# Performance work log

Measured on AMD Instinct MI355X. Metric: run time of the kernel, lower is better.

## Reference

```python
import jax, jax.numpy as jnp
import numpy as np

E = 192; Q = 48; H = 3; HD = Q // H  # per-branch embed 48, 3 heads of 16
CONV_CH = 4; K = 15; PAD = K // 2


def layer_norm(x, g, b, eps=1e-6):
    m = jnp.mean(x, axis=-1, keepdims=True)
    v = jnp.mean((x - m) ** 2, axis=-1, keepdims=True)
    return (x - m) * jax.lax.rsqrt(v + eps) * g + b


def mha(x, w_in, b_in, w_o, b_o):
    # x: [B,S,48]; torch nn.MultiheadAttention math (dropout=eval/identity)
    B, S, _ = x.shape
    qkv = x @ w_in.T + b_in                      # [B,S,144]
    q, k, v = jnp.split(qkv, 3, axis=-1)
    q = q.reshape(B, S, H, HD)
    k = k.reshape(B, S, H, HD)
    v = v.reshape(B, S, H, HD)
    scores = jnp.einsum('bqhd,bkhd->bhqk', q, k) / jnp.sqrt(jnp.float32(HD))
    attn = jax.nn.softmax(scores, axis=-1)
    out = jnp.einsum('bhqk,bkhd->bqhd', attn, v).reshape(B, S, Q)
    return out @ w_o.T + b_o


def light_conv(x96, conv_w):
    # x96: [B,S,96] -> view(-1, 4, 96), depthwise conv1d (k=15, pad=7), view back
    B, S, W = x96.shape
    r = x96.reshape(-1, CONV_CH, W)              # [B*S/... wait: B*S*96/(4*96)=B*S/4? No: reshape(-1,4,96) => [B*S, ...]
    y = jax.lax.conv_general_dilated(
        r, conv_w, window_strides=(1,), padding=[(PAD, PAD)],
        dimension_numbers=('NCH', 'OIH', 'NCH'), feature_group_count=CONV_CH)
    return y.reshape(B, S, W)


def setup_inputs() -> dict:
    key = jax.random.key(0)
    ks = jax.random.split(key, 16)
    sc = 0.05
    d = {
        'x': jax.random.normal(ks[0], (128, 512, E), dtype=jnp.float32),
        'ln1_g': jnp.ones((E,), jnp.float32), 'ln1_b': jnp.zeros((E,), jnp.float32),
        'acc_wqkv': jax.random.normal(ks[1], (3 * Q, Q), jnp.float32) * sc,
        'acc_bqkv': jnp.zeros((3 * Q,), jnp.float32),
        'acc_wo': jax.random.normal(ks[2], (Q, Q), jnp.float32) * sc,
        'acc_bo': jnp.zeros((Q,), jnp.float32),
        'gyro_wqkv': jax.random.normal(ks[3], (3 * Q, Q), jnp.float32) * sc,
        'gyro_bqkv': jnp.zeros((3 * Q,), jnp.float32),
        'gyro_wo': jax.random.normal(ks[4], (Q, Q), jnp.float32) * sc,
        'gyro_bo': jnp.zeros((Q,), jnp.float32),
        'conv_w': jax.random.normal(ks[5], (CONV_CH, 1, K), jnp.float32) * sc,
        'ln2_g': jnp.ones((E,), jnp.float32), 'ln2_b': jnp.zeros((E,), jnp.float32),
        'w1': jax.random.normal(ks[6], (2 * E, E), jnp.float32) * sc,
        'b1': jnp.zeros((2 * E,), jnp.float32),
        'w2': jax.random.normal(ks[7], (E, 2 * E), jnp.float32) * sc,
        'b2': jnp.zeros((E,), jnp.float32),
    }
    return d


def reference(x, ln1_g, ln1_b, acc_wqkv, acc_bqkv, acc_wo, acc_bo,
              gyro_wqkv, gyro_bqkv, gyro_wo, gyro_bo, conv_w,
              ln2_g, ln2_b, w1, b1, w2, b2):
    xn = layer_norm(x, ln1_g, ln1_b)
    x_conv = light_conv(xn[:, :, 48:144], conv_w)
    x_acc = mha(xn[:, :, 0:48], acc_wqkv, acc_bqkv, acc_wo, acc_bo)
    x_gyro = mha(xn[:, :, 96:144], gyro_wqkv, gyro_bqkv, gyro_wo, gyro_bo)
    xcat = jnp.concatenate([x_acc, x_conv, x_gyro], axis=2)
    x1 = xcat + x
    tt = layer_norm(x1, ln2_g, ln2_b)
    tt = jax.nn.relu(tt @ w1.T + b1)
    tt = jax.nn.relu(tt @ w2.T + b2)
    return x1 + tt
```

## Files before the change

kernel.cpp:

```cpp
#include <hip/hip_runtime.h>
#include <stdint.h>

typedef unsigned short u16;
typedef short bf16x8 __attribute__((ext_vector_type(8)));
typedef float f32x4 __attribute__((ext_vector_type(4)));
typedef float f32x16 __attribute__((ext_vector_type(16)));
typedef uint32_t u32x4 __attribute__((ext_vector_type(4)));

#define NB   128
#define SEQ  512
#define EMB  192
#define NTOK (NB * SEQ)
#define F1DIM 384
#define ATTW 128
#define VTP  520
#define KTS  24
#define XnS  200
#define X1S  196
#define H1S  392

__device__ __forceinline__ float bf2f(u16 u) {
  union { uint32_t u; float f; } v; v.u = ((uint32_t)u) << 16; return v.f;
}
__device__ __forceinline__ u16 f2bf(float f) {
  union { float f; uint32_t u; } v; v.f = f;
  uint32_t r = v.u + 0x7fffu + ((v.u >> 16) & 1u);
  return (u16)(r >> 16);
}
__device__ __forceinline__ uint32_t pack2bf(float a, float b) {
  return (uint32_t)f2bf(a) | ((uint32_t)f2bf(b) << 16);
}

__global__ __launch_bounds__(256) void pack_kernel(const float* __restrict__ w1,
    const float* __restrict__ w2, const float* __restrict__ wqa,
    const float* __restrict__ wqg, const float* __restrict__ woa,
    const float* __restrict__ wog, u16* __restrict__ w1b, u16* __restrict__ w2b,
    u16* __restrict__ wqp, u16* __restrict__ wop) {
  int idx = (int)blockIdx.x * 256 + (int)threadIdx.x;
  if (idx < 73728) {
    w1b[idx] = f2bf(w1[idx]);
  } else if (idx < 147456) {
    w2b[idx - 73728] = f2bf(w2[idx - 73728]);
  } else if (idx < 165888) {
    int i = idx - 147456;
    int row = i >> 6, k = i & 63;
    float v = 0.0f;
    if (k < 48) v = (row < 144) ? wqa[row * 48 + k] : wqg[(row - 144) * 48 + k];
    wqp[i] = f2bf(v);
  } else if (idx < 172032) {
    int i = idx - 165888;
    int row = i >> 6, k = i & 63;
    float v = 0.0f;
    if (k < 48) v = (row < 48) ? woa[row * 48 + k] : wog[(row - 48) * 48 + k];
    wop[i] = f2bf(v);
  }
}

__global__ __launch_bounds__(256) void ln1_qkv_conv_kernel(
    const float* __restrict__ x, const float* __restrict__ g,
    const float* __restrict__ b, const u16* __restrict__ wq,
    const float* __restrict__ bacc, const float* __restrict__ bgyr,
    const float* __restrict__ cw, u16* __restrict__ qkv,
    float* __restrict__ out) {
  __shared__ u16 Xn[64 * XnS];
  int bm = (int)blockIdx.x * 64;
  int tid = threadIdx.x;
  int trow = tid >> 2, part = tid & 3;
  int tok = bm + trow;
  const float* xr = x + (size_t)tok * EMB + part * 48;
  float vals[48];
#pragma unroll
  for (int j = 0; j < 48; j += 4) {
    float4 v = *(const float4*)(xr + j);
    vals[j] = v.x; vals[j + 1] = v.y; vals[j + 2] = v.z; vals[j + 3] = v.w;
  }
  float s = 0.0f, s2 = 0.0f;
#pragma unroll
  for (int j = 0; j < 48; j++) { s += vals[j]; s2 += vals[j] * vals[j]; }
  s += __shfl_xor(s, 1); s2 += __shfl_xor(s2, 1);
  s += __shfl_xor(s, 2); s2 += __shfl_xor(s2, 2);
  float mean = s * (1.0f / EMB);
  float var  = s2 * (1.0f / EMB) - mean * mean;
  float rs   = rsqrtf(var + 1e-6f);
  {
    u16* xnrow = Xn + trow * XnS + part * 48;
    const float* gp = g + part * 48;
    const float* bp = b + part * 48;
#pragma unroll
    for (int j = 0; j < 48; j += 2) {
      uint32_t w = pack2bf((vals[j] - mean) * rs * gp[j] + bp[j],
                           (vals[j + 1] - mean) * rs * gp[j + 1] + bp[j + 1]);
      *(uint32_t*)(xnrow + j) = w;
    }
  }
  __syncthreads();
  int wid = tid >> 6, lane = tid & 63;
  int l15 = lane & 15, quad = lane >> 4;
  const u16* arow_l = Xn + (wid * 16 + l15) * XnS;
  f32x4 acc[18] = {};
#pragma unroll
  for (int ks = 0; ks < 2; ks++) {
    int kk = ks * 32;
    bf16x8 af_a = *(const bf16x8*)(arow_l + kk + quad * 8);
    bf16x8 af_g = *(const bf16x8*)(arow_l + 96 + kk + quad * 8);
#pragma unroll
    for (int st = 0; st < 18; st++) {
      bf16x8 bf = *(const bf16x8*)(wq + (size_t)(st * 16 + l15) * 64 + kk + quad * 8);
      acc[st] = __builtin_amdgcn_mfma_f32_16x16x32_bf16(st < 9 ? af_a : af_g,
                                                        bf, acc[st], 0, 0, 0);
    }
  }
#pragma unroll
  for (int st = 0; st < 18; st++) {
    int col = st * 16 + l15;
    int cc = (col < 144) ? col : col - 144;
    float bias = (col < 144) ? bacc[cc] : bgyr[cc];
    float qs = (cc < 48) ? 0.36067376022f : 1.0f;
#pragma unroll
    for (int r = 0; r < 4; r++) {
      int orow = bm + wid * 16 + quad * 4 + r;
      qkv[(size_t)orow * 288 + col] = f2bf((acc[st][r] + bias) * qs);
    }
  }
  {
    int wr = trow & 3;
    float w15[15];
#pragma unroll
    for (int k = 0; k < 15; k++) w15[k] = cw[wr * 15 + k];
    float win[38];
    int base = part * 24 - 7;
#pragma unroll
    for (int i = 0; i < 38; i++) {
      int p = base + i;
      win[i] = (p >= 0 && p < 96) ? bf2f(Xn[trow * XnS + 48 + p]) : 0.0f;
    }
    const float* xres = x + (size_t)tok * EMB + 48 + part * 24;
    float* orow = out + (size_t)tok * EMB + 48 + part * 24;
#pragma unroll
    for (int c = 0; c < 24; c += 4) {
      float4 r4 = *(const float4*)(xres + c);
      float o[4];
#pragma unroll
      for (int u = 0; u < 4; u++) {
        float sc = 0.0f;
#pragma unroll
        for (int k = 0; k < 15; k++) sc += win[c + u + k] * w15[k];
        o[u] = sc;
      }
      float4 st4 = { o[0] + r4.x, o[1] + r4.y, o[2] + r4.z, o[3] + r4.w };
      *(float4*)(orow + c) = st4;
    }
  }
}

__global__ __launch_bounds__(256) void attn_kernel(const u16* __restrict__ qkv,
                                                   u16* __restrict__ att) {
  __shared__ u16 Kt[SEQ * KTS];
  __shared__ u16 Vt[17 * VTP];
  int bid = blockIdx.x;
  int hh  = bid % 3;
  int brb = (bid / 3) & 1;
  int b   = bid / 6;
  int tid = threadIdx.x;
  size_t tokbase = (size_t)b * SEQ;
  int qoff = brb * 144 + hh * 16;
  int koff = qoff + 48;
  int voff = qoff + 96;
  for (int r = tid; r < SEQ; r += 256) {
    const u16* src = qkv + (tokbase + r) * 288;
    *(uint4*)(Kt + r * KTS)     = *(const uint4*)(src + koff);
    *(uint4*)(Kt + r * KTS + 8) = *(const uint4*)(src + koff + 8);
    u16 tmp[16];
    *(uint4*)(tmp)     = *(const uint4*)(src + voff);
    *(uint4*)(tmp + 8) = *(const uint4*)(src + voff + 8);
#pragma unroll
    for (int j = 0; j < 16; j++) Vt[j * VTP + r] = tmp[j];
  }
  Vt[16 * VTP + tid]       = 0x3F80;
  Vt[16 * VTP + 256 + tid] = 0x3F80;
  __syncthreads();
  int wave = tid >> 6, lane = tid & 63;
  int q31 = lane & 31, h = lane >> 5;
  int dcl = (q31 < 16) ? q31 : 16;
#pragma unroll 1
  for (int qi = 0; qi < 4; qi++) {
    int qrow = (wave * 4 + qi) * 32 + q31;
    bf16x8 qfrag = *(const bf16x8*)(qkv + (tokbase + qrow) * 288 + qoff + h * 8);
    f32x16 Ot = {};
#pragma unroll 2
    for (int kt = 0; kt < 16; kt++) {
      bf16x8 kfrag = *(const bf16x8*)(Kt + (kt * 32 + q31) * KTS + h * 8);
      f32x16 zc = {};
      f32x16 S = __builtin_amdgcn_mfma_f32_32x32x16_bf16(kfrag, qfrag, zc, 0, 0, 0);
      uint32_t pk[8], swk[8];
#pragma unroll
      for (int i = 0; i < 8; i++) {
        union { float f; uint32_t u; } a0, a1;
        a0.f = exp2f(S[2 * i]);
        a1.f = exp2f(S[2 * i + 1]);
        pk[i] = __builtin_amdgcn_perm(a1.u, a0.u, 0x07060302u);
        swk[i] = (uint32_t)__shfl_xor((int)pk[i], 32);
      }
      u32x4 t1 = { h ? swk[2] : pk[0], h ? swk[3] : pk[1],
                   h ? pk[2]  : swk[0], h ? pk[3]  : swk[1] };
      u32x4 t2 = { h ? swk[6] : pk[4], h ? swk[7] : pk[5],
                   h ? pk[6]  : swk[4], h ? pk[7]  : swk[5] };
      bf16x8 pb1 = __builtin_bit_cast(bf16x8, t1);
      bf16x8 pb2 = __builtin_bit_cast(bf16x8, t2);
      bf16x8 av1 = *(const bf16x8*)(Vt + dcl * VTP + kt * 32 + h * 8);
      bf16x8 av2 = *(const bf16x8*)(Vt + dcl * VTP + kt * 32 + 16 + h * 8);
      Ot = __builtin_amdgcn_mfma_f32_32x32x16_bf16(av1, pb1, Ot, 0, 0, 0);
      Ot = __builtin_amdgcn_mfma_f32_32x32x16_bf16(av2, pb2, Ot, 0, 0, 0);
    }
    float inv = 1.0f / Ot[8];
    u16* orow = att + (tokbase + qrow) * ATTW + brb * 48 + hh * 16 + 4 * h;
    uint2 st0 = { pack2bf(Ot[0] * inv, Ot[1] * inv),
                  pack2bf(Ot[2] * inv, Ot[3] * inv) };
    uint2 st1 = { pack2bf(Ot[4] * inv, Ot[5] * inv),
                  pack2bf(Ot[6] * inv, Ot[7] * inv) };
    *(uint2*)(orow)     = st0;
    *(uint2*)(orow + 8) = st1;
  }
}

__global__ __launch_bounds__(256) void outproj_ln2_kernel(
    const u16* __restrict__ att, const u16* __restrict__ wo,
    const float* __restrict__ boacc, const float* __restrict__ bogyr,
    const float* __restrict__ x, const float* __restrict__ g2,
    const float* __restrict__ b2v, float* __restrict__ out,
    u16* __restrict__ tn) {
  __shared__ float X1[64 * X1S];
  int bm = (int)blockIdx.x * 64;
  int tid = threadIdx.x;
  int trow = tid >> 2, part = tid & 3;
  {
    const float* src = out + (size_t)(bm + trow) * EMB + 48 + part * 24;
    float* dst = X1 + trow * X1S + 48 + part * 24;
#pragma unroll
    for (int c = 0; c < 24; c += 4) *(float4*)(dst + c) = *(const float4*)(src + c);
  }
  int wid = tid >> 6, lane = tid & 63;
  int l15 = lane & 15, quad = lane >> 4;
  int row = bm + wid * 16 + l15;
  const u16* arow = att + (size_t)row * ATTW;
  f32x4 acc[6] = {};
#pragma unroll
  for (int ks = 0; ks < 2; ks++) {
    int kk = ks * 32;
    bf16x8 af_a = *(const bf16x8*)(arow + kk + quad * 8);
    bf16x8 af_g = *(const bf16x8*)(arow + 48 + kk + quad * 8);
#pragma unroll
    for (int st = 0; st < 6; st++) {
      bf16x8 bf = *(const bf16x8*)(wo + (size_t)(st * 16 + l15) * 64 + kk + quad * 8);
      acc[st] = __builtin_amdgcn_mfma_f32_16x16x32_bf16(st < 3 ? af_a : af_g,
                                                        bf, acc[st], 0, 0, 0);
    }
  }
#pragma unroll
  for (int st = 0; st < 6; st++) {
    int col = st * 16 + l15;
    float bias = (col < 48) ? boacc[col] : bogyr[col - 48];
    int oc = (col < 48) ? col : col + 96;
#pragma unroll
    for (int r = 0; r < 4; r++) {
      int lrow = wid * 16 + quad * 4 + r;
      size_t oi = (size_t)(bm + lrow) * EMB + oc;
      float v = acc[st][r] + bias + x[oi];
      out[oi] = v;
      X1[lrow * X1S + oc] = v;
    }
  }
  __syncthreads();
  const float* xl = X1 + trow * X1S + part * 48;
  float vals[48];
#pragma unroll
  for (int j = 0; j < 48; j += 4) {
    float4 v = *(const float4*)(xl + j);
    vals[j] = v.x; vals[j + 1] = v.y; vals[j + 2] = v.z; vals[j + 3] = v.w;
  }
  float s = 0.0f, s2 = 0.0f;
#pragma unroll
  for (int j = 0; j < 48; j++) { s += vals[j]; s2 += vals[j] * vals[j]; }
  s += __shfl_xor(s, 1); s2 += __shfl_xor(s2, 1);
  s += __shfl_xor(s, 2); s2 += __shfl_xor(s2, 2);
  float mean = s * (1.0f / EMB);
  float var  = s2 * (1.0f / EMB) - mean * mean;
  float rs   = rsqrtf(var + 1e-6f);
  u16* trp = tn + (size_t)(bm + trow) * EMB + part * 48;
  const float* gp = g2 + part * 48;
  const float* bp = b2v + part * 48;
#pragma unroll
  for (int j = 0; j < 48; j += 2) {
    uint32_t w = pack2bf((vals[j] - mean) * rs * gp[j] + bp[j],
                         (vals[j + 1] - mean) * rs * gp[j + 1] + bp[j + 1]);
    *(uint32_t*)(trp + j) = w;
  }
}

__global__ __launch_bounds__(256) void ffn_kernel(const u16* __restrict__ tn,
    const u16* __restrict__ w1b, const float* __restrict__ b1,
    const u16* __restrict__ w2b, const float* __restrict__ b2,
    float* __restrict__ out) {
  __shared__ u16 H1[64 * H1S];
  int bm = (int)blockIdx.x * 64;
  int tid = threadIdx.x;
  int wid = tid >> 6, lane = tid & 63;
  int l15 = lane & 15, quad = lane >> 4;
  f32x4 acc[24] = {};
#pragma unroll
  for (int kk = 0; kk < 192; kk += 32) {
    bf16x8 a0 = *(const bf16x8*)(tn + (size_t)(bm + 0 * 16 + l15) * EMB + kk + quad * 8);
    bf16x8 a1 = *(const bf16x8*)(tn + (size_t)(bm + 1 * 16 + l15) * EMB + kk + quad * 8);
    bf16x8 a2 = *(const bf16x8*)(tn + (size_t)(bm + 2 * 16 + l15) * EMB + kk + quad * 8);
    bf16x8 a3 = *(const bf16x8*)(tn + (size_t)(bm + 3 * 16 + l15) * EMB + kk + quad * 8);
#pragma unroll
    for (int stl = 0; stl < 6; stl++) {
      bf16x8 bf = *(const bf16x8*)(w1b + (size_t)((wid * 6 + stl) * 16 + l15) * EMB + kk + quad * 8);
      acc[0 * 6 + stl] = __builtin_amdgcn_mfma_f32_16x16x32_bf16(a0, bf, acc[0 * 6 + stl], 0, 0, 0);
      acc[1 * 6 + stl] = __builtin_amdgcn_mfma_f32_16x16x32_bf16(a1, bf, acc[1 * 6 + stl], 0, 0, 0);
      acc[2 * 6 + stl] = __builtin_amdgcn_mfma_f32_16x16x32_bf16(a2, bf, acc[2 * 6 + stl], 0, 0, 0);
      acc[3 * 6 + stl] = __builtin_amdgcn_mfma_f32_16x16x32_bf16(a3, bf, acc[3 * 6 + stl], 0, 0, 0);
    }
  }
#pragma unroll
  for (int stl = 0; stl < 6; stl++) {
    int col = (wid * 6 + stl) * 16 + l15;
    float bias = b1[col];
#pragma unroll
    for (int m = 0; m < 4; m++) {
#pragma unroll
      for (int r = 0; r < 4; r++) {
        float v = acc[m * 6 + stl][r] + bias;
        v = v > 0.0f ? v : 0.0f;
        H1[(m * 16 + quad * 4 + r) * H1S + col] = f2bf(v);
      }
    }
  }
  __syncthreads();
  f32x4 acc2[12] = {};
#pragma unroll
  for (int kk = 0; kk < 384; kk += 32) {
    bf16x8 a0 = *(const bf16x8*)(H1 + (0 * 16 + l15) * H1S + kk + quad * 8);
    bf16x8 a1 = *(const bf16x8*)(H1 + (1 * 16 + l15) * H1S + kk + quad * 8);
    bf16x8 a2 = *(const bf16x8*)(H1 + (2 * 16 + l15) * H1S + kk + quad * 8);
    bf16x8 a3 = *(const bf16x8*)(H1 + (3 * 16 + l15) * H1S + kk + quad * 8);
#pragma unroll
    for (int stl = 0; stl < 3; stl++) {
      bf16x8 bf = *(const bf16x8*)(w2b + (size_t)((wid * 3 + stl) * 16 + l15) * F1DIM + kk + quad * 8);
      acc2[0 * 3 + stl] = __builtin_amdgcn_mfma_f32_16x16x32_bf16(a0, bf, acc2[0 * 3 + stl], 0, 0, 0);
      acc2[1 * 3 + stl] = __builtin_amdgcn_mfma_f32_16x16x32_bf16(a1, bf, acc2[1 * 3 + stl], 0, 0, 0);
      acc2[2 * 3 + stl] = __builtin_amdgcn_mfma_f32_16x16x32_bf16(a2, bf, acc2[2 * 3 + stl], 0, 0, 0);
      acc2[3 * 3 + stl] = __builtin_amdgcn_mfma_f32_16x16x32_bf16(a3, bf, acc2[3 * 3 + stl], 0, 0, 0);
    }
  }
#pragma unroll
  for (int stl = 0; stl < 3; stl++) {
    int col = (wid * 3 + stl) * 16 + l15;
    float bias = b2[col];
#pragma unroll
    for (int m = 0; m < 4; m++) {
#pragma unroll
      for (int r = 0; r < 4; r++) {
        size_t oi = (size_t)(bm + m * 16 + quad * 4 + r) * EMB + col;
        float v = acc2[m * 3 + stl][r] + bias;
        v = v > 0.0f ? v : 0.0f;
        out[oi] = out[oi] + v;
      }
    }
  }
}

extern "C" void kernel_launch(void* const* d_in, const int* in_sizes, int n_in,
                              void* d_out, int out_size, void* d_ws, size_t ws_size,
                              hipStream_t stream) {
  const float* x         = (const float*)d_in[0];
  const float* ln1_g     = (const float*)d_in[1];
  const float* ln1_b     = (const float*)d_in[2];
  const float* acc_wqkv  = (const float*)d_in[3];
  const float* acc_bqkv  = (const float*)d_in[4];
  const float* acc_wo    = (const float*)d_in[5];
  const float* acc_bo    = (const float*)d_in[6];
  const float* gyro_wqkv = (const float*)d_in[7];
  const float* gyro_bqkv = (const float*)d_in[8];
  const float* gyro_wo   = (const float*)d_in[9];
  const float* gyro_bo   = (const float*)d_in[10];
  const float* conv_w    = (const float*)d_in[11];
  const float* ln2_g     = (const float*)d_in[12];
  const float* ln2_b     = (const float*)d_in[13];
  const float* w1        = (const float*)d_in[14];
  const float* b1        = (const float*)d_in[15];
  const float* w2        = (const float*)d_in[16];
  const float* b2        = (const float*)d_in[17];
  float* out = (float*)d_out;
  char* ws = (char*)d_ws;

  u16* qkvb = (u16*)(ws);
  u16* attb = (u16*)(ws + 37748736);
  u16* tn   = (u16*)(ws + 54525952);
  u16* w1b  = (u16*)(ws + 79691776);
  u16* w2b  = (u16*)(ws + 79839232);
  u16* wqp  = (u16*)(ws + 79986688);
  u16* wop  = (u16*)(ws + 80023552);

  pack_kernel<<<672, 256, 0, stream>>>(w1, w2, acc_wqkv, gyro_wqkv, acc_wo,
                                       gyro_wo, w1b, w2b, wqp, wop);
  ln1_qkv_conv_kernel<<<NTOK / 64, 256, 0, stream>>>(
      x, ln1_g, ln1_b, wqp, acc_bqkv, gyro_bqkv, conv_w, qkvb, out);
  attn_kernel<<<NB * 6, 256, 0, stream>>>(qkvb, attb);
  outproj_ln2_kernel<<<NTOK / 64, 256, 0, stream>>>(
      attb, wop, acc_bo, gyro_bo, x, ln2_g, ln2_b, out, tn);
  ffn_kernel<<<NTOK / 64, 256, 0, stream>>>(tn, w1b, b1, w2b, b2, out);
}
```

Baseline: 346.5 us.

## Fuse out-projection, LayerNorm2 and FFN into one 512-thread tail kernel

Merges the outproj+LN2 kernel and the FFN kernel into one kernel that keeps the normalized activations in shared memory instead of writing and rereading a bf16 buffer in global memory. The block grows to 512 threads (8 waves), and the out-projection and both FFN GEMMs are split across 2x4 wave groups. The H1 buffer reuses the X1 shared region after a barrier. This removes a launch and the global round trip of the tn tensor, at the cost of more shared memory per block and extra barriers.

```diff
diff --git a/kernel.cpp b/kernel.cpp
--- a/kernel.cpp
+++ b/kernel.cpp
@@ -223,148 +223,146 @@
   }
 }
 
-__global__ __launch_bounds__(256) void outproj_ln2_kernel(
+__global__ __launch_bounds__(512) void tail_kernel(
     const u16* __restrict__ att, const u16* __restrict__ wo,
     const float* __restrict__ boacc, const float* __restrict__ bogyr,
     const float* __restrict__ x, const float* __restrict__ g2,
-    const float* __restrict__ b2v, float* __restrict__ out,
-    u16* __restrict__ tn) {
+    const float* __restrict__ b2v, const u16* __restrict__ w1b,
+    const float* __restrict__ b1, const u16* __restrict__ w2b,
+    const float* __restrict__ b2, float* __restrict__ out) {
   __shared__ float X1[64 * X1S];
-  int bm = (int)blockIdx.x * 64;
-  int tid = threadIdx.x;
-  int trow = tid >> 2, part = tid & 3;
-  {
-    const float* src = out + (size_t)(bm + trow) * EMB + 48 + part * 24;
-    float* dst = X1 + trow * X1S + 48 + part * 24;
-#pragma unroll
-    for (int c = 0; c < 24; c += 4) *(float4*)(dst + c) = *(const float4*)(src + c);
-  }
-  int wid = tid >> 6, lane = tid & 63;
-  int l15 = lane & 15, quad = lane >> 4;
-  int row = bm + wid * 16 + l15;
-  const u16* arow = att + (size_t)row * ATTW;
-  f32x4 acc[6] = {};
-#pragma unroll
-  for (int ks = 0; ks < 2; ks++) {
-    int kk = ks * 32;
-    bf16x8 af_a = *(const bf16x8*)(arow + kk + quad * 8);
-    bf16x8 af_g = *(const bf16x8*)(arow + 48 + kk + quad * 8);
-#pragma unroll
-    for (int st = 0; st < 6; st++) {
-      bf16x8 bf = *(const bf16x8*)(wo + (size_t)(st * 16 + l15) * 64 + kk + quad * 8);
-      acc[st] = __builtin_amdgcn_mfma_f32_16x16x32_bf16(st < 3 ? af_a : af_g,
-                                                        bf, acc[st], 0, 0, 0);
-    }
-  }
-#pragma unroll
-  for (int st = 0; st < 6; st++) {
-    int col = st * 16 + l15;
-    float bias = (col < 48) ? boacc[col] : bogyr[col - 48];
-    int oc = (col < 48) ? col : col + 96;
-#pragma unroll
-    for (int r = 0; r < 4; r++) {
-      int lrow = wid * 16 + quad * 4 + r;
-      size_t oi = (size_t)(bm + lrow) * EMB + oc;
-      float v = acc[st][r] + bias + x[oi];
-      out[oi] = v;
-      X1[lrow * X1S + oc] = v;
-    }
-  }
-  __syncthreads();
-  const float* xl = X1 + trow * X1S + part * 48;
-  float vals[48];
-#pragma unroll
-  for (int j = 0; j < 48; j += 4) {
-    float4 v = *(const float4*)(xl + j);
-    vals[j] = v.x; vals[j + 1] = v.y; vals[j + 2] = v.z; vals[j + 3] = v.w;
-  }
-  float s = 0.0f, s2 = 0.0f;
-#pragma unroll
-  for (int j = 0; j < 48; j++) { s += vals[j]; s2 += vals[j] * vals[j]; }
-  s += __shfl_xor(s, 1); s2 += __shfl_xor(s2, 1);
-  s += __shfl_xor(s, 2); s2 += __shfl_xor(s2, 2);
-  float mean = s * (1.0f / EMB);
-  float var  = s2 * (1.0f / EMB) - mean * mean;
-  float rs   = rsqrtf(var + 1e-6f);
-  u16* trp = tn + (size_t)(bm + trow) * EMB + part * 48;
-  const float* gp = g2 + part * 48;
-  const float* bp = b2v + part * 48;
-#pragma unroll
-  for (int j = 0; j < 48; j += 2) {
-    uint32_t w = pack2bf((vals[j] - mean) * rs * gp[j] + bp[j],
-                         (vals[j + 1] - mean) * rs * gp[j + 1] + bp[j + 1]);
-    *(uint32_t*)(trp + j) = w;
-  }
-}
-
-__global__ __launch_bounds__(256) void ffn_kernel(const u16* __restrict__ tn,
-    const u16* __restrict__ w1b, const float* __restrict__ b1,
-    const u16* __restrict__ w2b, const float* __restrict__ b2,
-    float* __restrict__ out) {
-  __shared__ u16 H1[64 * H1S];
+  __shared__ u16 Tn[64 * XnS];
+  u16* H1 = (u16*)X1;
   int bm = (int)blockIdx.x * 64;
   int tid = threadIdx.x;
   int wid = tid >> 6, lane = tid & 63;
   int l15 = lane & 15, quad = lane >> 4;
-  f32x4 acc[24] = {};
-#pragma unroll
-  for (int kk = 0; kk < 192; kk += 32) {
-    bf16x8 a0 = *(const bf16x8*)(tn + (size_t)(bm + 0 * 16 + l15) * EMB + kk + quad * 8);
-    bf16x8 a1 = *(const bf16x8*)(tn + (size_t)(bm + 1 * 16 + l15) * EMB + kk + quad * 8);
-    bf16x8 a2 = *(const bf16x8*)(tn + (size_t)(bm + 2 * 16 + l15) * EMB + kk + quad * 8);
-    bf16x8 a3 = *(const bf16x8*)(tn + (size_t)(bm + 3 * 16 + l15) * EMB + kk + quad * 8);
+  if (tid < 256) {
+    int trow = tid >> 2, part = tid & 3;
+    const float* src = out + (size_t)(bm + trow) * EMB + 48 + part * 24;
+    float* dst = X1 + trow * X1S + 48 + part * 24;
+#pragma unroll
+    for (int c = 0; c < 24; c += 4) *(float4*)(dst + c) = *(const float4*)(src + c);
+  }
+  {
+    int mt = wid & 3, ng = wid >> 2;
+    int row = bm + mt * 16 + l15;
+    const u16* arow = att + (size_t)row * ATTW + (ng ? 48 : 0);
+    f32x4 acc[3] = {};
+#pragma unroll
+    for (int ks = 0; ks < 2; ks++) {
+      int kk = ks * 32;
+      bf16x8 af = *(const bf16x8*)(arow + kk + quad * 8);
+#pragma unroll
+      for (int st = 0; st < 3; st++) {
+        int stg = ng * 3 + st;
+        bf16x8 bf = *(const bf16x8*)(wo + (size_t)(stg * 16 + l15) * 64 + kk + quad * 8);
+        acc[st] = __builtin_amdgcn_mfma_f32_16x16x32_bf16(af, bf, acc[st], 0, 0, 0);
+      }
+    }
+#pragma unroll
+    for (int st = 0; st < 3; st++) {
+      int col = (ng * 3 + st) * 16 + l15;
+      float bias = (col < 48) ? boacc[col] : bogyr[col - 48];
+      int oc = (col < 48) ? col : col + 96;
+#pragma unroll
+      for (int r = 0; r < 4; r++) {
+        int lrow = mt * 16 + quad * 4 + r;
+        size_t oi = (size_t)(bm + lrow) * EMB + oc;
+        float v = acc[st][r] + bias + x[oi];
+        out[oi] = v;
+        X1[lrow * X1S + oc] = v;
+      }
+    }
+  }
+  __syncthreads();
+  {
+    int trow = tid >> 3, part = tid & 7;
+    const float* xl = X1 + trow * X1S + part * 24;
+    float vals[24];
+#pragma unroll
+    for (int j = 0; j < 24; j += 4) {
+      float4 v = *(const float4*)(xl + j);
+      vals[j] = v.x; vals[j + 1] = v.y; vals[j + 2] = v.z; vals[j + 3] = v.w;
+    }
+    float s = 0.0f, s2 = 0.0f;
+#pragma unroll
+    for (int j = 0; j < 24; j++) { s += vals[j]; s2 += vals[j] * vals[j]; }
+    s += __shfl_xor(s, 1); s2 += __shfl_xor(s2, 1);
+    s += __shfl_xor(s, 2); s2 += __shfl_xor(s2, 2);
+    s += __shfl_xor(s, 4); s2 += __shfl_xor(s2, 4);
+    float mean = s * (1.0f / EMB);
+    float var  = s2 * (1.0f / EMB) - mean * mean;
+    float rs   = rsqrtf(var + 1e-6f);
+    u16* trp = Tn + trow * XnS + part * 24;
+    const float* gp = g2 + part * 24;
+    const float* bp = b2v + part * 24;
+#pragma unroll
+    for (int j = 0; j < 24; j += 2) {
+      uint32_t w = pack2bf((vals[j] - mean) * rs * gp[j] + bp[j],
+                           (vals[j + 1] - mean) * rs * gp[j + 1] + bp[j + 1]);
+      *(uint32_t*)(trp + j) = w;
+    }
+  }
+  __syncthreads();
+  {
+    int mg = wid & 1, ng = wid >> 1;
+    f32x4 acc1[12] = {};
+#pragma unroll
+    for (int kk = 0; kk < 192; kk += 32) {
+      bf16x8 a0 = *(const bf16x8*)(Tn + (mg * 32 + l15) * XnS + kk + quad * 8);
+      bf16x8 a1 = *(const bf16x8*)(Tn + (mg * 32 + 16 + l15) * XnS + kk + quad * 8);
+#pragma unroll
+      for (int stl = 0; stl < 6; stl++) {
+        bf16x8 bf = *(const bf16x8*)(w1b + (size_t)((ng * 6 + stl) * 16 + l15) * EMB + kk + quad * 8);
+        acc1[stl]     = __builtin_amdgcn_mfma_f32_16x16x32_bf16(a0, bf, acc1[stl], 0, 0, 0);
+        acc1[6 + stl] = __builtin_amdgcn_mfma_f32_16x16x32_bf16(a1, bf, acc1[6 + stl], 0, 0, 0);
+      }
+    }
+    __syncthreads();
 #pragma unroll
     for (int stl = 0; stl < 6; stl++) {
-      bf16x8 bf = *(const bf16x8*)(w1b + (size_t)((wid * 6 + stl) * 16 + l15) * EMB + kk + quad * 8);
-      acc[0 * 6 + stl] = __builtin_amdgcn_mfma_f32_16x16x32_bf16(a0, bf, acc[0 * 6 + stl], 0, 0, 0);
-      acc[1 * 6 + stl] = __builtin_amdgcn_mfma_f32_16x16x32_bf16(a1, bf, acc[1 * 6 + stl], 0, 0, 0);
-      acc[2 * 6 + stl] = __builtin_amdgcn_mfma_f32_16x16x32_bf16(a2, bf, acc[2 * 6 + stl], 0, 0, 0);
-      acc[3 * 6 + stl] = __builtin_amdgcn_mfma_f32_16x16x32_bf16(a3, bf, acc[3 * 6 + stl], 0, 0, 0);
-    }
-  }
-#pragma unroll
-  for (int stl = 0; stl < 6; stl++) {
-    int col = (wid * 6 + stl) * 16 + l15;
-    float bias = b1[col];
-#pragma unroll
-    for (int m = 0; m < 4; m++) {
-#pragma unroll
-      for (int r = 0; r < 4; r++) {
-        float v = acc[m * 6 + stl][r] + bias;
-        v = v > 0.0f ? v : 0.0f;
-        H1[(m * 16 + quad * 4 + r) * H1S + col] = f2bf(v);
+      int col = (ng * 6 + stl) * 16 + l15;
+      float bias = b1[col];
+#pragma unroll
+      for (int m2 = 0; m2 < 2; m2++) {
+#pragma unroll
+        for (int r = 0; r < 4; r++) {
+          float v = acc1[m2 * 6 + stl][r] + bias;
+          v = v > 0.0f ? v : 0.0f;
+          H1[(mg * 32 + m2 * 16 + quad * 4 + r) * H1S + col] = f2bf(v);
+        }
       }
     }
   }
   __syncthreads();
-  f32x4 acc2[12] = {};
-#pragma unroll
-  for (int kk = 0; kk < 384; kk += 32) {
-    bf16x8 a0 = *(const bf16x8*)(H1 + (0 * 16 + l15) * H1S + kk + quad * 8);
-    bf16x8 a1 = *(const bf16x8*)(H1 + (1 * 16 + l15) * H1S + kk + quad * 8);
-    bf16x8 a2 = *(const bf16x8*)(H1 + (2 * 16 + l15) * H1S + kk + quad * 8);
-    bf16x8 a3 = *(const bf16x8*)(H1 + (3 * 16 + l15) * H1S + kk + quad * 8);
+  {
+    int mg2 = wid & 1, ng2 = wid >> 1;
+    f32x4 acc2[6] = {};
+#pragma unroll
+    for (int kk = 0; kk < 384; kk += 32) {
+      bf16x8 a0 = *(const bf16x8*)(H1 + (mg2 * 32 + l15) * H1S + kk + quad * 8);
+      bf16x8 a1 = *(const bf16x8*)(H1 + (mg2 * 32 + 16 + l15) * H1S + kk + quad * 8);
+#pragma unroll
+      for (int stl = 0; stl < 3; stl++) {
+        bf16x8 bf = *(const bf16x8*)(w2b + (size_t)((ng2 * 3 + stl) * 16 + l15) * F1DIM + kk + quad * 8);
+        acc2[stl]     = __builtin_amdgcn_mfma_f32_16x16x32_bf16(a0, bf, acc2[stl], 0, 0, 0);
+        acc2[3 + stl] = __builtin_amdgcn_mfma_f32_16x16x32_bf16(a1, bf, acc2[3 + stl], 0, 0, 0);
+      }
+    }
 #pragma unroll
     for (int stl = 0; stl < 3; stl++) {
-      bf16x8 bf = *(const bf16x8*)(w2b + (size_t)((wid * 3 + stl) * 16 + l15) * F1DIM + kk + quad * 8);
-      acc2[0 * 3 + stl] = __builtin_amdgcn_mfma_f32_16x16x32_bf16(a0, bf, acc2[0 * 3 + stl], 0, 0, 0);
-      acc2[1 * 3 + stl] = __builtin_amdgcn_mfma_f32_16x16x32_bf16(a1, bf, acc2[1 * 3 + stl], 0, 0, 0);
-      acc2[2 * 3 + stl] = __builtin_amdgcn_mfma_f32_16x16x32_bf16(a2, bf, acc2[2 * 3 + stl], 0, 0, 0);
-      acc2[3 * 3 + stl] = __builtin_amdgcn_mfma_f32_16x16x32_bf16(a3, bf, acc2[3 * 3 + stl], 0, 0, 0);
-    }
-  }
-#pragma unroll
-  for (int stl = 0; stl < 3; stl++) {
-    int col = (wid * 3 + stl) * 16 + l15;
-    float bias = b2[col];
-#pragma unroll
-    for (int m = 0; m < 4; m++) {
-#pragma unroll
-      for (int r = 0; r < 4; r++) {
-        size_t oi = (size_t)(bm + m * 16 + quad * 4 + r) * EMB + col;
-        float v = acc2[m * 3 + stl][r] + bias;
-        v = v > 0.0f ? v : 0.0f;
-        out[oi] = out[oi] + v;
+      int col = (ng2 * 3 + stl) * 16 + l15;
+      float bias = b2[col];
+#pragma unroll
+      for (int m2 = 0; m2 < 2; m2++) {
+#pragma unroll
+        for (int r = 0; r < 4; r++) {
+          size_t oi = (size_t)(bm + mg2 * 32 + m2 * 16 + quad * 4 + r) * EMB + col;
+          float v = acc2[m2 * 3 + stl][r] + bias;
+          v = v > 0.0f ? v : 0.0f;
+          out[oi] = out[oi] + v;
+        }
       }
     }
   }
@@ -396,18 +394,16 @@
 
   u16* qkvb = (u16*)(ws);
   u16* attb = (u16*)(ws + 37748736);
-  u16* tn   = (u16*)(ws + 54525952);
-  u16* w1b  = (u16*)(ws + 79691776);
-  u16* w2b  = (u16*)(ws + 79839232);
-  u16* wqp  = (u16*)(ws + 79986688);
-  u16* wop  = (u16*)(ws + 80023552);
+  u16* w1b  = (u16*)(ws + 54525952);
+  u16* w2b  = (u16*)(ws + 54673408);
+  u16* wqp  = (u16*)(ws + 54820864);
+  u16* wop  = (u16*)(ws + 54857728);
 
   pack_kernel<<<672, 256, 0, stream>>>(w1, w2, acc_wqkv, gyro_wqkv, acc_wo,
                                        gyro_wo, w1b, w2b, wqp, wop);
   ln1_qkv_conv_kernel<<<NTOK / 64, 256, 0, stream>>>(
       x, ln1_g, ln1_b, wqp, acc_bqkv, gyro_bqkv, conv_w, qkvb, out);
   attn_kernel<<<NB * 6, 256, 0, stream>>>(qkvb, attb);
-  outproj_ln2_kernel<<<NTOK / 64, 256, 0, stream>>>(
-      attb, wop, acc_bo, gyro_bo, x, ln2_g, ln2_b, out, tn);
-  ffn_kernel<<<NTOK / 64, 256, 0, stream>>>(tn, w1b, b1, w2b, b2, out);
-}
+  tail_kernel<<<NTOK / 64, 512, 0, stream>>>(
+      attb, wop, acc_bo, gyro_bo, x, ln2_g, ln2_b, w1b, b1, w2b, b2, out);
+}
```

New measurement: 327.4 us. 1.06x faster.
